# Kernel optimization log

Hardware: AMD Instinct MI355X
Metric: run time of the kernel (lower is better)

## Reference

```python
import jax, jax.numpy as jnp
import numpy as np

N_NODES = 50000
N_EDGES = 800000
N_FEAT = 128
N_GRAPHS = 512
OUT_DIM = 128


def gcn_conv(x, W, b, src, dst, ew, n):
    """PyG GCNConv: h = x @ W; add self-loops (weight 1); symmetric norm
    D^-1/2 A D^-1/2 with edge weights; scatter-add messages src->dst; + bias."""
    h = x @ W  # [n, out]
    loop = jnp.arange(n)
    s = jnp.concatenate([src, loop])
    d = jnp.concatenate([dst, loop])
    w = jnp.concatenate([ew, jnp.ones((n,), x.dtype)])
    deg = jax.ops.segment_sum(w, d, num_segments=n)
    dinv = jnp.where(deg > 0, jax.lax.rsqrt(deg), 0.0)
    norm = dinv[s] * w * dinv[d]  # [E+n]
    out = jax.ops.segment_sum(h[s] * norm[:, None], d, num_segments=n)
    return out + b


def setup_inputs() -> dict:
    key = jax.random.key(0)
    ks = jax.random.split(key, 12)
    F = N_FEAT
    x = jax.random.normal(ks[0], (N_NODES, F), jnp.float32)
    edge_index = jax.random.randint(ks[1], (2, N_EDGES), 0, N_NODES, jnp.int64)
    edge_attr = jax.random.uniform(ks[2], (N_EDGES,), jnp.float32)
    # deterministic sorted graph assignment -> no empty graphs (avoids -inf in max pool)
    batch = (jnp.arange(N_NODES, dtype=jnp.int64) * N_GRAPHS) // N_NODES
    def lin(k, fi, fo):
        s = 1.0 / np.sqrt(fi)
        return jax.random.uniform(k, (fi, fo), jnp.float32, -s, s)
    return {
        "x": x, "edge_attr": edge_attr,
        "W1": lin(ks[3], F, F), "b1": jnp.zeros((F,), jnp.float32),
        "W2": lin(ks[4], F, 2 * F), "b2": jnp.zeros((2 * F,), jnp.float32),
        "W3": lin(ks[5], 2 * F, 4 * F), "b3": jnp.zeros((4 * F,), jnp.float32),
        "Wf1": lin(ks[6], 4 * F, 1024), "bf1": jnp.zeros((1024,), jnp.float32),
        "Wf2": lin(ks[7], 1024, OUT_DIM), "bf2": jnp.zeros((OUT_DIM,), jnp.float32),
        "edge_index": edge_index, "batch": batch,
    }


def reference(x, edge_attr, W1, b1, W2, b2, W3, b3, Wf1, bf1, Wf2, bf2,
              edge_index, batch):
    n = x.shape[0]
    src, dst = edge_index[0], edge_index[1]
    h = jax.nn.relu(gcn_conv(x, W1, b1, src, dst, edge_attr, n))
    h = jax.nn.relu(gcn_conv(h, W2, b2, src, dst, edge_attr, n))
    h = jax.nn.relu(gcn_conv(h, W3, b3, src, dst, edge_attr, n))
    # global max pool over nodes per graph
    g = jax.ops.segment_max(h, batch, num_segments=N_GRAPHS)  # [G, 4F]
    g = jax.nn.relu(g @ Wf1 + bf1)
    # dropout is identity in eval mode
    out = g @ Wf2 + bf2
    return out
```

## Files before the change

### kernel.cpp

```cpp
#include <hip/hip_runtime.h>

#define NNODES 50000
#define NPAD   50048
#define NEDGES 800000
#define NGRAPH 512
#define DCAP 64

typedef short bf16x8 __attribute__((ext_vector_type(8)));
typedef unsigned short u16x8 __attribute__((ext_vector_type(8)));
typedef float f32x4 __attribute__((ext_vector_type(4)));
typedef unsigned long long u64;

#define GLOAD16(g, l)                                                                 \
    __builtin_amdgcn_global_load_lds((const __attribute__((address_space(1))) unsigned*)(g), \
                                     (__attribute__((address_space(3))) unsigned*)(l), 16, 0, 0)

static __device__ __forceinline__ float b2f(unsigned short u) {
    return __uint_as_float(((unsigned)u) << 16);
}
static __device__ __forceinline__ unsigned short f2b(float f) {
    unsigned u = __float_as_uint(f);
    unsigned r = (u + 0x7fffu + ((u >> 16) & 1u)) >> 16;
    return (unsigned short)r;
}

static __device__ __forceinline__ void accum8(float (&acc)[8], float c, uint4 v) {
    unsigned w[4] = {v.x, v.y, v.z, v.w};
    #pragma unroll
    for (int i = 0; i < 4; ++i) {
        acc[2 * i]     += c * __uint_as_float(w[i] << 16);
        acc[2 * i + 1] += c * __uint_as_float(w[i] & 0xffff0000u);
    }
}

__global__ __launch_bounds__(256) void k_init(const float* __restrict__ W1, const float* __restrict__ W2,
                                              const float* __restrict__ W3, const float* __restrict__ Wf1,
                                              const float* __restrict__ Wf2,
                                              unsigned short* __restrict__ T1, unsigned short* __restrict__ T2,
                                              unsigned short* __restrict__ T3, unsigned short* __restrict__ Tf1,
                                              unsigned short* __restrict__ Tf2,
                                              u64* deg_cnt, int* gp) {
    int i = blockIdx.x * 256 + threadIdx.x;
    if (i < NNODES) deg_cnt[i] = (u64)(1u << 24);
    if (i < NGRAPH * 512) gp[i] = 0;

    const int b = blockIdx.x;
    if (b >= 204) return;
    const float* W; unsigned short* T; int K, N, t0;
    if (b < 4)        { W = W1;  T = T1;  K = 128;  N = 128;  t0 = 0;   }
    else if (b < 12)  { W = W2;  T = T2;  K = 128;  N = 256;  t0 = 4;   }
    else if (b < 44)  { W = W3;  T = T3;  K = 256;  N = 512;  t0 = 12;  }
    else if (b < 172) { W = Wf1; T = Tf1; K = 512;  N = 1024; t0 = 44;  }
    else              { W = Wf2; T = Tf2; K = 1024; N = 128;  t0 = 172; }
    const int tile = b - t0;
    const int ntn = N >> 6;
    const int k0 = (tile / ntn) * 64, n0 = (tile % ntn) * 64;
    __shared__ float sm[64][65];
    const int t = threadIdx.x;
    const int rr = t >> 6, cc = t & 63;
    #pragma unroll
    for (int r = 0; r < 16; ++r) {
        int kl = r * 4 + rr;
        sm[kl][cc] = W[(size_t)(k0 + kl) * N + n0 + cc];
    }
    __syncthreads();
    #pragma unroll
    for (int r = 0; r < 16; ++r) {
        int nl = r * 4 + rr;
        T[(size_t)(n0 + nl) * K + k0 + cc] = f2b(sm[cc][nl]);
    }
}

__global__ __launch_bounds__(256) void k_count(const int4* __restrict__ ei_s,
                                               const int4* __restrict__ ei_d,
                                               const float4* __restrict__ ew4,
                                               u64* deg_cnt,
                                               unsigned* __restrict__ edges) {
    int t = blockIdx.x * 256 + threadIdx.x;
    if (t >= NEDGES / 4) return;
    int4 ss = ei_s[t];
    int4 dd = ei_d[t];
    float4 ww = ew4[t];
    int s[4] = {ss.x, ss.y, ss.z, ss.w};
    int d[4] = {dd.x, dd.y, dd.z, dd.w};
    float w[4] = {ww.x, ww.y, ww.z, ww.w};
    int slot[4];
    #pragma unroll
    for (int u = 0; u < 4; ++u) {
        unsigned fixed = __float2uint_rn(w[u] * 16777216.0f);
        u64 old = atomicAdd(&deg_cnt[d[u]], ((u64)1 << 32) | fixed);
        slot[u] = (int)(old >> 32);
        if (slot[u] > DCAP - 1) slot[u] = DCAP - 1;
    }
    #pragma unroll
    for (int u = 0; u < 4; ++u)
        edges[((unsigned)d[u] << 6) | slot[u]] = ((unsigned)f2b(w[u]) << 16) | (unsigned)s[u];
}

__global__ void k_prep(const u64* __restrict__ deg_cnt, float* __restrict__ dinv) {
    int i = blockIdx.x * 256 + threadIdx.x;
    if (i < NNODES)
        dinv[i] = rsqrtf((float)(unsigned)(deg_cnt[i] & 0xffffffffull) * 5.9604645e-8f);
}

__global__ void k_cvt4(const float* __restrict__ X, const float* __restrict__ dinv,
                       unsigned short* __restrict__ Y, int n4) {
    int i = blockIdx.x * 256 + threadIdx.x;
    if (i < n4) {
        float4 v = ((const float4*)X)[i];
        float d = dinv[i >> 5];
        uint2 o;
        o.x = (unsigned)f2b(v.x * d) | ((unsigned)f2b(v.y * d) << 16);
        o.y = (unsigned)f2b(v.z * d) | ((unsigned)f2b(v.w * d) << 16);
        ((uint2*)Y)[i] = o;
    }
}

template <int F>
__global__ __launch_bounds__(256) void k_aggregate(const unsigned short* __restrict__ X,
                                                   const u64* __restrict__ deg_cnt,
                                                   const unsigned* __restrict__ edges,
                                                   const float* __restrict__ dinv,
                                                   unsigned short* __restrict__ Z) {
    constexpr int LPR = F / 8;
    constexpr int GRP = 64 / LPR;
    constexpr int STEP = GRP * 2;
    const int wave = threadIdx.x >> 6, lane = threadIdx.x & 63;
    const int node = blockIdx.x * 4 + wave;
    if (node >= NNODES) return;
    const int sub = lane & (LPR - 1);
    const int grp = lane / LPR;
    const int fo = sub * 8;
    const unsigned short* Xf = X + fo;
    const float di = dinv[node];
    const int cnt = (int)(deg_cnt[node] >> 32);
    const unsigned* erow = edges + ((unsigned)node << 6);

    const uint4 selfv = *(const uint4*)(Xf + (size_t)node * F);

    float acc[8] = {};

    const int e0 = grp;
    const int nb = (cnt + STEP - 1) / STEP;

    unsigned pa0 = 0, pb0 = 0, pa1 = 0, pb1 = 0;
    uint4 va0 = {}, vb0 = {};
    if (nb > 0) {
        int ea = e0, eb = e0 + GRP;
        pa0 = (ea < cnt) ? erow[ea] : 0u;
        pb0 = (eb < cnt) ? erow[eb] : 0u;
        va0 = *(const uint4*)(Xf + (size_t)(pa0 & 0xffffu) * F);
        vb0 = *(const uint4*)(Xf + (size_t)(pb0 & 0xffffu) * F);
        if (nb > 1) {
            int ea1 = e0 + STEP, eb1 = ea1 + GRP;
            pa1 = (ea1 < cnt) ? erow[ea1] : 0u;
            pb1 = (eb1 < cnt) ? erow[eb1] : 0u;
        }
    }
    for (int p = 0; p < nb; ++p) {
        uint4 va1 = {}, vb1 = {};
        unsigned pa2 = 0, pb2 = 0;
        if (p + 1 < nb) {
            va1 = *(const uint4*)(Xf + (size_t)(pa1 & 0xffffu) * F);
            vb1 = *(const uint4*)(Xf + (size_t)(pb1 & 0xffffu) * F);
            if (p + 2 < nb) {
                int ea = e0 + (p + 2) * STEP, eb = ea + GRP;
                pa2 = (ea < cnt) ? erow[ea] : 0u;
                pb2 = (eb < cnt) ? erow[eb] : 0u;
            }
        }
        accum8(acc, b2f((unsigned short)(pa0 >> 16)), va0);
        accum8(acc, b2f((unsigned short)(pb0 >> 16)), vb0);
        pa0 = pa1; pb0 = pb1; va0 = va1; vb0 = vb1;
        pa1 = pa2; pb1 = pb2;
    }

    #pragma unroll
    for (int j = 0; j < 8; ++j) {
        if constexpr (GRP == 4) acc[j] += __shfl_xor(acc[j], 16, 64);
        acc[j] += __shfl_xor(acc[j], 32, 64);
    }

    if (grp == 0) {
        unsigned w[4] = {selfv.x, selfv.y, selfv.z, selfv.w};
        unsigned o[4];
        #pragma unroll
        for (int i = 0; i < 4; ++i) {
            float s0 = __uint_as_float(w[i] << 16);
            float s1 = __uint_as_float(w[i] & 0xffff0000u);
            unsigned short c0 = f2b(di * (acc[2 * i] + s0));
            unsigned short c1 = f2b(di * (acc[2 * i + 1] + s1));
            o[i] = (unsigned)c0 | ((unsigned)c1 << 16);
        }
        uint4 ov; ov.x = o[0]; ov.y = o[1]; ov.z = o[2]; ov.w = o[3];
        *(uint4*)(Z + (size_t)node * F + fo) = ov;
    }
}

template <int CMODE>
__global__ __launch_bounds__(256) void k_gemm128(const unsigned short* __restrict__ A,
                                                 const unsigned short* __restrict__ WT,
                                                 const float* __restrict__ bias,
                                                 unsigned short* __restrict__ C,
                                                 const int* __restrict__ batch,
                                                 int* __restrict__ gp,
                                                 const float* __restrict__ rscale,
                                                 int M, int N, int K) {
    __shared__ unsigned short As[128 * 32];
    __shared__ unsigned short Bs[128 * 32];
    const int tid = threadIdx.x;

    const int nwg = gridDim.x * gridDim.y;
    const int f = blockIdx.y * gridDim.x + blockIdx.x;
    const int q = nwg >> 3, r = nwg & 7;
    const int xcd = f & 7, idx = f >> 3;
    const int w = (xcd < r) ? xcd * (q + 1) + idx : r * (q + 1) + (xcd - r) * q + idx;
    const int m0 = (w / gridDim.x) * 128;
    const int n0 = (w % gridDim.x) * 128;

    const int wave = tid >> 6, lane = tid & 63;
    const int wm = (wave >> 1) * 64, wn = (wave & 1) * 64;
    const int quad = lane >> 4, mrow = lane & 15;

    const int sr = tid >> 2;
    const int sc = (tid & 3) * 8;
    const unsigned short* Ag0 = A + (size_t)(m0 + sr) * K + sc;
    const unsigned short* Ag1 = A + (size_t)(m0 + 64 + sr) * K + sc;
    const unsigned short* Bg0 = WT + (size_t)(n0 + sr) * K + sc;
    const unsigned short* Bg1 = WT + (size_t)(n0 + 64 + sr) * K + sc;
    unsigned short* Ad0 = &As[sr * 32 + sc];
    unsigned short* Ad1 = &As[(64 + sr) * 32 + sc];
    unsigned short* Bd0 = &Bs[sr * 32 + sc];
    unsigned short* Bd1 = &Bs[(64 + sr) * 32 + sc];

    f32x4 acc[4][4] = {};

    for (int k0 = 0; k0 < K; k0 += 32) {
        GLOAD16(Ag0 + k0, Ad0);
        GLOAD16(Ag1 + k0, Ad1);
        GLOAD16(Bg0 + k0, Bd0);
        GLOAD16(Bg1 + k0, Bd1);
        __syncthreads();
        bf16x8 af[4], bf[4];
        #pragma unroll
        for (int mt = 0; mt < 4; ++mt)
            af[mt] = *(const bf16x8*)&As[(wm + mt * 16 + mrow) * 32 + quad * 8];
        #pragma unroll
        for (int nt = 0; nt < 4; ++nt)
            bf[nt] = *(const bf16x8*)&Bs[(wn + nt * 16 + mrow) * 32 + quad * 8];
        #pragma unroll
        for (int mt = 0; mt < 4; ++mt)
            #pragma unroll
            for (int nt = 0; nt < 4; ++nt)
                acc[mt][nt] = __builtin_amdgcn_mfma_f32_16x16x32_bf16(af[mt], bf[nt], acc[mt][nt], 0, 0, 0);
        __syncthreads();
    }

    float bn[4];
    #pragma unroll
    for (int nt = 0; nt < 4; ++nt) bn[nt] = bias[n0 + wn + nt * 16 + mrow];

    if constexpr (CMODE == 0) {
        #pragma unroll
        for (int mt = 0; mt < 4; ++mt) {
            #pragma unroll
            for (int r4 = 0; r4 < 4; ++r4) {
                int row = m0 + wm + mt * 16 + quad * 4 + r4;
                if (row < M) {
                    float rs = rscale ? rscale[row] : 1.0f;
                    #pragma unroll
                    for (int nt = 0; nt < 4; ++nt) {
                        float v = fmaxf(acc[mt][nt][r4] + bn[nt], 0.f) * rs;
                        C[(size_t)row * N + n0 + wn + nt * 16 + mrow] = f2b(v);
                    }
                }
            }
        }
    } else {
        const int wr0 = m0 + wm;
        int g0i = wr0 < M ? wr0 : M - 1;
        const int g0 = batch[g0i];
        int lastr = wr0 + 63; if (lastr >= M) lastr = M - 1;
        const int gl = batch[lastr];
        bool rok[16]; int gid[16];
        #pragma unroll
        for (int mt = 0; mt < 4; ++mt)
            #pragma unroll
            for (int r4 = 0; r4 < 4; ++r4) {
                int row = wr0 + mt * 16 + quad * 4 + r4;
                rok[mt * 4 + r4] = row < M;
                gid[mt * 4 + r4] = (row < M) ? batch[row] : -1;
            }
        #pragma unroll
        for (int nt = 0; nt < 4; ++nt) {
            float v0 = 0.f, v1 = 0.f;
            #pragma unroll
            for (int mt = 0; mt < 4; ++mt)
                #pragma unroll
                for (int r4 = 0; r4 < 4; ++r4)
                    if (rok[mt * 4 + r4]) {
                        float v = fmaxf(acc[mt][nt][r4] + bn[nt], 0.f);
                        if (gid[mt * 4 + r4] == g0) v0 = fmaxf(v0, v);
                        else v1 = fmaxf(v1, v);
                    }
            v0 = fmaxf(v0, __shfl_xor(v0, 16, 64));
            v0 = fmaxf(v0, __shfl_xor(v0, 32, 64));
            v1 = fmaxf(v1, __shfl_xor(v1, 16, 64));
            v1 = fmaxf(v1, __shfl_xor(v1, 32, 64));
            if (quad == 0) {
                int c = n0 + wn + nt * 16 + mrow;
                atomicMax(&gp[(size_t)g0 * N + c], __float_as_int(v0));
                if (gl != g0) atomicMax(&gp[(size_t)gl * N + c], __float_as_int(v1));
            }
        }
    }
}

template <int CMODE, int AFP>
__global__ __launch_bounds__(256) void k_gemm_mfma(const void* __restrict__ Av,
                                                   const unsigned short* __restrict__ WT,
                                                   const float* __restrict__ bias,
                                                   void* __restrict__ Cv,
                                                   int M, int N, int K) {
    constexpr int LDK = 40;
    __shared__ unsigned short As[64 * LDK];
    __shared__ unsigned short Bs[128 * LDK];
    const int tid = threadIdx.x;
    const int m0 = blockIdx.y * 64, n0 = blockIdx.x * 128;
    const int wave = tid >> 6, lane = tid & 63;
    const int wm = (wave >> 1) * 32;
    const int wn = (wave & 1) * 64;
    const int quad = lane >> 4, mrow = lane & 15;

    const int ar = tid >> 2;
    const int ak = (tid & 3) * 8;
    const bool arow_ok = (m0 + ar) < M;
    const size_t aoff = (size_t)(m0 + ar) * K + ak;
    const unsigned short* Bg0 = WT + (size_t)(n0 + ar) * K + ak;
    const unsigned short* Bg1 = WT + (size_t)(n0 + ar + 64) * K + ak;

    f32x4 acc[2][4] = {};

    for (int k0 = 0; k0 < K; k0 += 32) {
        u16x8 av = {};
        if (arow_ok) {
            if constexpr (AFP) {
                const float* Af = (const float*)Av + aoff + k0;
                float4 f0 = *(const float4*)Af;
                float4 f1 = *(const float4*)(Af + 4);
                av[0] = (short)f2b(f0.x); av[1] = (short)f2b(f0.y);
                av[2] = (short)f2b(f0.z); av[3] = (short)f2b(f0.w);
                av[4] = (short)f2b(f1.x); av[5] = (short)f2b(f1.y);
                av[6] = (short)f2b(f1.z); av[7] = (short)f2b(f1.w);
            } else {
                av = *(const u16x8*)((const unsigned short*)Av + aoff + k0);
            }
        }
        u16x8 bv0 = *(const u16x8*)(Bg0 + k0);
        u16x8 bv1 = *(const u16x8*)(Bg1 + k0);
        *(u16x8*)&As[ar * LDK + ak] = av;
        *(u16x8*)&Bs[ar * LDK + ak] = bv0;
        *(u16x8*)&Bs[(ar + 64) * LDK + ak] = bv1;
        __syncthreads();
        bf16x8 af[2], bf[4];
        #pragma unroll
        for (int mt = 0; mt < 2; ++mt)
            af[mt] = *(const bf16x8*)&As[(wm + mt * 16 + mrow) * LDK + quad * 8];
        #pragma unroll
        for (int nt = 0; nt < 4; ++nt)
            bf[nt] = *(const bf16x8*)&Bs[(wn + nt * 16 + mrow) * LDK + quad * 8];
        #pragma unroll
        for (int mt = 0; mt < 2; ++mt)
            #pragma unroll
            for (int nt = 0; nt < 4; ++nt)
                acc[mt][nt] = __builtin_amdgcn_mfma_f32_16x16x32_bf16(af[mt], bf[nt], acc[mt][nt], 0, 0, 0);
        __syncthreads();
    }

    float bn[4];
    #pragma unroll
    for (int nt = 0; nt < 4; ++nt) bn[nt] = bias[n0 + wn + nt * 16 + mrow];

    if constexpr (CMODE == 0) {
        unsigned short* C = (unsigned short*)Cv;
        #pragma unroll
        for (int mt = 0; mt < 2; ++mt) {
            #pragma unroll
            for (int r = 0; r < 4; ++r) {
                int row = m0 + wm + mt * 16 + quad * 4 + r;
                if (row < M) {
                    #pragma unroll
                    for (int nt = 0; nt < 4; ++nt) {
                        float v = fmaxf(acc[mt][nt][r] + bn[nt], 0.f);
                        C[(size_t)row * N + n0 + wn + nt * 16 + mrow] = f2b(v);
                    }
                }
            }
        }
    } else {
        float* C = (float*)Cv;
        #pragma unroll
        for (int mt = 0; mt < 2; ++mt) {
            #pragma unroll
            for (int r = 0; r < 4; ++r) {
                int row = m0 + wm + mt * 16 + quad * 4 + r;
                if (row < M) {
                    #pragma unroll
                    for (int nt = 0; nt < 4; ++nt)
                        C[(size_t)row * N + n0 + wn + nt * 16 + mrow] = acc[mt][nt][r] + bn[nt];
                }
            }
        }
    }
}

extern "C" void kernel_launch(void* const* d_in, const int* in_sizes, int n_in,
                              void* d_out, int out_size, void* d_ws, size_t ws_size,
                              hipStream_t stream) {
    const float* x   = (const float*)d_in[0];
    const float* ew  = (const float*)d_in[1];
    const float* W1  = (const float*)d_in[2];
    const float* b1  = (const float*)d_in[3];
    const float* W2  = (const float*)d_in[4];
    const float* b2  = (const float*)d_in[5];
    const float* W3  = (const float*)d_in[6];
    const float* b3  = (const float*)d_in[7];
    const float* Wf1 = (const float*)d_in[8];
    const float* bf1 = (const float*)d_in[9];
    const float* Wf2 = (const float*)d_in[10];
    const float* bf2 = (const float*)d_in[11];
    const int* ei    = (const int*)d_in[12];
    const int* batch = (const int*)d_in[13];
    float* out = (float*)d_out;
    (void)in_sizes; (void)n_in; (void)out_size; (void)ws_size;

    char* p = (char*)d_ws;
    auto alloc = [&](size_t bytes) -> char* {
        char* r = p;
        p += (bytes + 255) & ~(size_t)255;
        return r;
    };
    const int nbN = (NNODES + 255) / 256;
    u64*   deg_cnt = (u64*)alloc((size_t)NNODES * 8);
    float* dinv   = (float*)alloc((size_t)NNODES * 4);
    unsigned* edges = (unsigned*)alloc((size_t)NNODES * DCAP * 4);
    int*   gp     = (int*)  alloc((size_t)NGRAPH * 512 * 4);
    unsigned short* f1   = (unsigned short*)alloc((size_t)NGRAPH * 1024 * 2);
    unsigned short* wt1  = (unsigned short*)alloc((size_t)128 * 128 * 2);
    unsigned short* wt2  = (unsigned short*)alloc((size_t)256 * 128 * 2);
    unsigned short* wt3  = (unsigned short*)alloc((size_t)512 * 256 * 2);
    unsigned short* wtf1 = (unsigned short*)alloc((size_t)1024 * 512 * 2);
    unsigned short* wtf2 = (unsigned short*)alloc((size_t)128 * 1024 * 2);
    unsigned short* bufA = (unsigned short*)alloc((size_t)NPAD * 256 * 2);
    unsigned short* bufB = (unsigned short*)alloc((size_t)NPAD * 256 * 2);
    unsigned short* x16  = bufB;

    const int MB128 = (NNODES + 127) / 128;
    const int AGG = (NNODES + 3) / 4;

    k_init<<<1024, 256, 0, stream>>>(W1, W2, W3, Wf1, Wf2,
                                     wt1, wt2, wt3, wtf1, wtf2, deg_cnt, gp);
    k_count<<<(NEDGES / 4 + 255) / 256, 256, 0, stream>>>(
        (const int4*)ei, (const int4*)(ei + NEDGES), (const float4*)ew, deg_cnt, edges);
    k_prep<<<nbN, 256, 0, stream>>>(deg_cnt, dinv);
    k_cvt4<<<(NNODES * 32 + 255) / 256, 256, 0, stream>>>(x, dinv, x16, NNODES * 32);

    k_aggregate<128><<<AGG, 256, 0, stream>>>(x16, deg_cnt, edges, dinv, bufA);
    k_gemm128<0><<<dim3(1, MB128), 256, 0, stream>>>(bufA, wt1, b1, bufB, nullptr, nullptr, dinv, NNODES, 128, 128);
    k_aggregate<128><<<AGG, 256, 0, stream>>>(bufB, deg_cnt, edges, dinv, bufA);
    k_gemm128<0><<<dim3(2, MB128), 256, 0, stream>>>(bufA, wt2, b2, bufB, nullptr, nullptr, dinv, NNODES, 256, 128);
    k_aggregate<256><<<AGG, 256, 0, stream>>>(bufB, deg_cnt, edges, dinv, bufA);
    k_gemm128<2><<<dim3(4, MB128), 256, 0, stream>>>(bufA, wt3, b3, nullptr, batch, gp, nullptr, NNODES, 512, 256);

    k_gemm_mfma<0, 1><<<dim3(8, NGRAPH / 64), 256, 0, stream>>>(gp, wtf1, bf1, f1, NGRAPH, 1024, 512);
    k_gemm_mfma<1, 0><<<dim3(1, NGRAPH / 64), 256, 0, stream>>>(f1, wtf2, bf2, out, NGRAPH, 128, 1024);
}
```

Before: 368.4 us.

## Double-buffer LDS tiles in node GEMM and fuse degree prep into conversion

The 128x128 MFMA GEMM now keeps two LDS buffers per operand. It issues the async global-to-LDS loads for the next K step before computing on the current one, so load latency can overlap the MFMAs. Separately, the rsqrt degree-normalization kernel is folded into the fp32-to-bf16 conversion kernel, removing one launch and the dinv round trip. In exchange, the GEMM's LDS use doubles, which may lower occupancy, and every conversion thread now recomputes the rsqrt redundantly.

```diff
diff --git a/kernel.cpp b/kernel.cpp
--- a/kernel.cpp
+++ b/kernel.cpp
@@ -97,18 +97,14 @@
         edges[((unsigned)d[u] << 6) | slot[u]] = ((unsigned)f2b(w[u]) << 16) | (unsigned)s[u];
 }
 
-__global__ void k_prep(const u64* __restrict__ deg_cnt, float* __restrict__ dinv) {
-    int i = blockIdx.x * 256 + threadIdx.x;
-    if (i < NNODES)
-        dinv[i] = rsqrtf((float)(unsigned)(deg_cnt[i] & 0xffffffffull) * 5.9604645e-8f);
-}
-
-__global__ void k_cvt4(const float* __restrict__ X, const float* __restrict__ dinv,
-                       unsigned short* __restrict__ Y, int n4) {
+__global__ void k_cvt_prep(const float* __restrict__ X, const u64* __restrict__ deg_cnt,
+                           float* __restrict__ dinv, unsigned short* __restrict__ Y, int n4) {
     int i = blockIdx.x * 256 + threadIdx.x;
     if (i < n4) {
+        int row = i >> 5;
+        float d = rsqrtf((float)(unsigned)(deg_cnt[row] & 0xffffffffull) * 5.9604645e-8f);
+        if ((i & 31) == 0) dinv[row] = d;
         float4 v = ((const float4*)X)[i];
-        float d = dinv[i >> 5];
         uint2 o;
         o.x = (unsigned)f2b(v.x * d) | ((unsigned)f2b(v.y * d) << 16);
         o.y = (unsigned)f2b(v.z * d) | ((unsigned)f2b(v.w * d) << 16);
@@ -206,8 +202,8 @@
                                                  int* __restrict__ gp,
                                                  const float* __restrict__ rscale,
                                                  int M, int N, int K) {
-    __shared__ unsigned short As[128 * 32];
-    __shared__ unsigned short Bs[128 * 32];
+    __shared__ unsigned short As[2][128 * 32];
+    __shared__ unsigned short Bs[2][128 * 32];
     const int tid = threadIdx.x;
 
     const int nwg = gridDim.x * gridDim.y;
@@ -228,26 +224,33 @@
     const unsigned short* Ag1 = A + (size_t)(m0 + 64 + sr) * K + sc;
     const unsigned short* Bg0 = WT + (size_t)(n0 + sr) * K + sc;
     const unsigned short* Bg1 = WT + (size_t)(n0 + 64 + sr) * K + sc;
-    unsigned short* Ad0 = &As[sr * 32 + sc];
-    unsigned short* Ad1 = &As[(64 + sr) * 32 + sc];
-    unsigned short* Bd0 = &Bs[sr * 32 + sc];
-    unsigned short* Bd1 = &Bs[(64 + sr) * 32 + sc];
+    const int so0 = sr * 32 + sc, so1 = (64 + sr) * 32 + sc;
 
     f32x4 acc[4][4] = {};
-
-    for (int k0 = 0; k0 < K; k0 += 32) {
-        GLOAD16(Ag0 + k0, Ad0);
-        GLOAD16(Ag1 + k0, Ad1);
-        GLOAD16(Bg0 + k0, Bd0);
-        GLOAD16(Bg1 + k0, Bd1);
-        __syncthreads();
+    const int nsteps = K >> 5;
+
+    GLOAD16(Ag0, &As[0][so0]);
+    GLOAD16(Ag1, &As[0][so1]);
+    GLOAD16(Bg0, &Bs[0][so0]);
+    GLOAD16(Bg1, &Bs[0][so1]);
+    __syncthreads();
+
+    for (int step = 0; step < nsteps; ++step) {
+        const int cur = step & 1;
+        if (step + 1 < nsteps) {
+            const int k1 = (step + 1) << 5;
+            GLOAD16(Ag0 + k1, &As[cur ^ 1][so0]);
+            GLOAD16(Ag1 + k1, &As[cur ^ 1][so1]);
+            GLOAD16(Bg0 + k1, &Bs[cur ^ 1][so0]);
+            GLOAD16(Bg1 + k1, &Bs[cur ^ 1][so1]);
+        }
         bf16x8 af[4], bf[4];
         #pragma unroll
         for (int mt = 0; mt < 4; ++mt)
-            af[mt] = *(const bf16x8*)&As[(wm + mt * 16 + mrow) * 32 + quad * 8];
+            af[mt] = *(const bf16x8*)&As[cur][(wm + mt * 16 + mrow) * 32 + quad * 8];
         #pragma unroll
         for (int nt = 0; nt < 4; ++nt)
-            bf[nt] = *(const bf16x8*)&Bs[(wn + nt * 16 + mrow) * 32 + quad * 8];
+            bf[nt] = *(const bf16x8*)&Bs[cur][(wn + nt * 16 + mrow) * 32 + quad * 8];
         #pragma unroll
         for (int mt = 0; mt < 4; ++mt)
             #pragma unroll
@@ -440,7 +443,6 @@
         p += (bytes + 255) & ~(size_t)255;
         return r;
     };
-    const int nbN = (NNODES + 255) / 256;
     u64*   deg_cnt = (u64*)alloc((size_t)NNODES * 8);
     float* dinv   = (float*)alloc((size_t)NNODES * 4);
     unsigned* edges = (unsigned*)alloc((size_t)NNODES * DCAP * 4);
@@ -462,8 +464,7 @@
                                      wt1, wt2, wt3, wtf1, wtf2, deg_cnt, gp);
     k_count<<<(NEDGES / 4 + 255) / 256, 256, 0, stream>>>(
         (const int4*)ei, (const int4*)(ei + NEDGES), (const float4*)ew, deg_cnt, edges);
-    k_prep<<<nbN, 256, 0, stream>>>(deg_cnt, dinv);
-    k_cvt4<<<(NNODES * 32 + 255) / 256, 256, 0, stream>>>(x, dinv, x16, NNODES * 32);
+    k_cvt_prep<<<(NNODES * 32 + 255) / 256, 256, 0, stream>>>(x, deg_cnt, dinv, x16, NNODES * 32);
 
     k_aggregate<128><<<AGG, 256, 0, stream>>>(x16, deg_cnt, edges, dinv, bufA);
     k_gemm128<0><<<dim3(1, MB128), 256, 0, stream>>>(bufA, wt1, b1, bufB, nullptr, nullptr, dinv, NNODES, 128, 128);
```

Result: no change. 365.4 us (-0.8%).
